# Kernel optimization log

Hardware: AMD Instinct MI355X
Metric: run time of the kernel (lower is better)

The kernel has to match this reference:

```python
import jax, jax.numpy as jnp
import numpy as np

HEAD_DIM = 64


def setup_inputs() -> dict:
    key = jax.random.key(0)
    ks = jax.random.split(key, 7)
    B, T, S = 8, 256, 4096
    E, KV = 512, 768          # embed_dim, kv_dim
    H, D = 8, HEAD_DIM        # num_heads, head_dim
    x = jax.random.normal(ks[0], (B, T, E), dtype=jnp.float32)
    context = jax.random.normal(ks[1], (B, S, KV), dtype=jnp.float32)
    key_padding_mask = jax.random.randint(ks[2], (B, S), 0, 2) > 0  # True = ignore
    Wq = jax.random.normal(ks[3], (H * D, E), dtype=jnp.float32) * 0.02
    Wkv = jax.random.normal(ks[4], (2 * H * D, KV), dtype=jnp.float32) * 0.02
    Wo = jax.random.normal(ks[5], (E, H * D), dtype=jnp.float32) * 0.02
    bo = jnp.zeros((E,), dtype=jnp.float32)
    return {"x": x, "context": context, "key_padding_mask": key_padding_mask,
            "Wq": Wq, "Wkv": Wkv, "Wo": Wo, "bo": bo}


def reference(x, context, key_padding_mask, Wq, Wkv, Wo, bo):
    B, T, _ = x.shape
    S = context.shape[1]
    D = HEAD_DIM
    H = Wq.shape[0] // D
    scale = D ** (-0.5)

    # q: (B, H, T, D)
    q = (x @ Wq.T).reshape(B, T, H, D).transpose(0, 2, 1, 3)
    # kv: (B, S, 2, H, D) -> k, v each (B, H, S, D)
    kv = (context @ Wkv.T).reshape(B, S, 2, H, D)
    k = kv[:, :, 0].transpose(0, 2, 1, 3)
    v = kv[:, :, 1].transpose(0, 2, 1, 3)

    # attention scores (B, H, T, S) -- materialized, matching att_weights capture
    attn = jnp.einsum('bhtd,bhsd->bhts', q, k) * scale
    attn = jnp.where(key_padding_mask[:, None, None, :], -jnp.inf, attn)
    attn = jax.nn.softmax(attn, axis=-1)  # dropout p=0.0 -> identity

    out = jnp.einsum('bhts,bhsd->bthd', attn, v).reshape(B, T, H * D)
    return out @ Wo.T + bo
```

## Files before the change

### kernel.cpp

```cpp
#include <hip/hip_runtime.h>
#include <hip/hip_bf16.h>


typedef float f32x4 __attribute__((ext_vector_type(4)));
typedef __bf16 bf16x8 __attribute__((ext_vector_type(8)));
typedef unsigned short u16x8 __attribute__((ext_vector_type(8)));
typedef unsigned short u16x4 __attribute__((ext_vector_type(4)));
typedef unsigned int u32x4 __attribute__((ext_vector_type(4)));

static __device__ __forceinline__ unsigned short f2bf(float f) {
  return __builtin_bit_cast(unsigned short, (__bf16)f);
}
static __device__ __forceinline__ unsigned pk2(float lo, float hi) {
  return (unsigned)f2bf(lo) | ((unsigned)f2bf(hi) << 16);
}
static __device__ __forceinline__ f32x4 mfma16(bf16x8 a, bf16x8 b, f32x4 c) {
  return __builtin_amdgcn_mfma_f32_16x16x32_bf16(a, b, c, 0, 0, 0);
}
static __device__ __forceinline__ bf16x8 ld_frag(const unsigned short* lds, int byteOff) {
  return __builtin_bit_cast(bf16x8, *(const u16x8*)((const char*)lds + byteOff));
}
static __device__ __forceinline__ void gll16(const void* g, void* l) {
  __builtin_amdgcn_global_load_lds((__attribute__((address_space(1))) void*)(void*)g,
                                   (__attribute__((address_space(3))) void*)l, 16, 0, 0);
}
static __device__ __forceinline__ int swz4(int row) {
  return (row + (row >> 1)) & 3;
}

__global__ __launch_bounds__(256) void cvt_ctx(const float* __restrict__ in,
                                               unsigned short* __restrict__ out) {
  const long t = blockIdx.x * 256L + threadIdx.x;
  f32x4 v[12];
#pragma unroll
  for (int it = 0; it < 6; ++it) {
    const f32x4* p = (const f32x4*)(in + (t + it * 524288L) * 8);
    v[it * 2] = p[0];
    v[it * 2 + 1] = p[1];
  }
#pragma unroll
  for (int it = 0; it < 6; ++it) {
    f32x4 a = v[it * 2], b = v[it * 2 + 1];
    u16x8 o = { f2bf(a[0]), f2bf(a[1]), f2bf(a[2]), f2bf(a[3]),
                f2bf(b[0]), f2bf(b[1]), f2bf(b[2]), f2bf(b[3]) };
    *(u16x8*)(out + (t + it * 524288L) * 8) = o;
  }
}

__global__ __launch_bounds__(256) void cvt_bf16(const float* __restrict__ in,
                                                unsigned short* __restrict__ out, int n8) {
  int i = blockIdx.x * 256 + threadIdx.x;
  if (i >= n8) return;
  const f32x4* p = (const f32x4*)(in + (long)i * 8);
  f32x4 a = p[0], b = p[1];
  u16x8 o = { f2bf(a[0]), f2bf(a[1]), f2bf(a[2]), f2bf(a[3]),
              f2bf(b[0]), f2bf(b[1]), f2bf(b[2]), f2bf(b[3]) };
  *(u16x8*)(out + (long)i * 8) = o;
}

__global__ __launch_bounds__(256) void gemm_kv(
    const unsigned short* __restrict__ A, const unsigned short* __restrict__ Bw,
    unsigned short* __restrict__ kbuf, unsigned short* __restrict__ vbuf) {
  constexpr int K = 768;
  constexpr int NT = K / 32;
  __shared__ unsigned short SH[24576];
  auto AsP = [&](int b) { return SH + b * 4096; };
  auto BsP = [&](int b) { return SH + 12288 + b * 4096; };
  const int tid = threadIdx.x;
  const int l = tid & 63, wid = tid >> 6;
  const int wr = wid >> 1, wc = wid & 1;
  const int r = l & 15, g = l >> 4;
  const int bid = blockIdx.x;
  const int xcd = bid & 7, j = bid >> 3;
  const long m0 = (long)(xcd * 32 + (j >> 3)) * 128;
  const long n0 = (long)(j & 7) * 128;

  const int row0 = tid >> 2, cs = tid & 3;
  const int gk0 = (cs ^ swz4(row0)) * 8;
  const unsigned short* aR = A + (m0 + row0) * K + gk0;
  const unsigned short* bR = Bw + (n0 + row0) * K + gk0;

  auto stage = [&](int sbuf, int kt) {
    const unsigned short* ap = aR + kt * 32;
    const unsigned short* bp = bR + kt * 32;
    gll16(ap,          (char*)AsP(sbuf) + tid * 16);
    gll16(ap + 64 * K, (char*)AsP(sbuf) + 4096 + tid * 16);
    gll16(bp,          (char*)BsP(sbuf) + tid * 16);
    gll16(bp + 64 * K, (char*)BsP(sbuf) + 4096 + tid * 16);
  };

  f32x4 acc[4][4] = {};
  stage(0, 0);
  stage(1, 1);
  asm volatile("s_waitcnt vmcnt(4)" ::: "memory");
  __builtin_amdgcn_s_barrier();
  __builtin_amdgcn_sched_barrier(0);

  int cur = 0, nxt2 = 2;
  for (int t = 0; t < NT; ++t) {
    if (t + 2 < NT) stage(nxt2, t + 2);
    bf16x8 af[4], bfr[4];
#pragma unroll
    for (int m = 0; m < 4; ++m) {
      int row = wr * 64 + m * 16 + r;
      af[m] = ld_frag(AsP(cur), row * 64 + ((g ^ swz4(row)) << 4));
    }
#pragma unroll
    for (int n = 0; n < 4; ++n) {
      int row = wc * 64 + n * 16 + r;
      bfr[n] = ld_frag(BsP(cur), row * 64 + ((g ^ swz4(row)) << 4));
    }
    __builtin_amdgcn_s_setprio(1);
#pragma unroll
    for (int m = 0; m < 4; ++m)
#pragma unroll
      for (int n = 0; n < 4; ++n)
        acc[m][n] = mfma16(af[m], bfr[n], acc[m][n]);
    __builtin_amdgcn_s_setprio(0);
    if (t + 2 < NT) {
      asm volatile("s_waitcnt vmcnt(4)" ::: "memory");
    } else {
      asm volatile("s_waitcnt vmcnt(0)" ::: "memory");
    }
    __builtin_amdgcn_s_barrier();
    __builtin_amdgcn_sched_barrier(0);
    cur = (cur == 2) ? 0 : cur + 1;
    nxt2 = (nxt2 == 2) ? 0 : nxt2 + 1;
  }

  const bool isK = (n0 < 512);
  unsigned short* ep = SH + wid * 4224;
#pragma unroll
  for (int m = 0; m < 4; ++m)
#pragma unroll
    for (int n = 0; n < 4; ++n)
#pragma unroll
      for (int i = 0; i < 4; ++i) {
        int lr = m * 16 + g * 4 + i;
        int lc = n * 16 + r;
        if (isK) ep[lr * 66 + lc] = f2bf(acc[m][n][i]);
        else     ep[lc * 66 + lr] = f2bf(acc[m][n][i]);
      }
  asm volatile("s_waitcnt lgkmcnt(0)" ::: "memory");

  const int rr0 = l >> 3, cch = l & 7;
  if (isK) {
    const int hh = (int)((n0 + wc * 64) >> 6);
    const long srow0 = m0 + wr * 64;
    const int bb = (int)(srow0 >> 12);
    unsigned short* kb = kbuf + ((long)(bb * 8 + hh) * 4096) * 64;
#pragma unroll
    for (int q = 0; q < 8; ++q) {
      int rr = q * 8 + rr0;
      u16x8 vv = *(const u16x8*)&ep[rr * 66 + cch * 8];
      int ss = (int)((srow0 + rr) & 4095);
      *(u16x8*)&kb[(long)ss * 64 + cch * 8] = vv;
    }
  } else {
    const int c2 = (int)(n0 - 512) + wc * 64;
    const int hh = c2 >> 6;
    const long srow0 = m0 + wr * 64;
    const int bb = (int)(srow0 >> 12), ss0 = (int)(srow0 & 4095);
    unsigned short* vb = vbuf + ((long)(bb * 8 + hh) * 64) * 4096;
#pragma unroll
    for (int q = 0; q < 8; ++q) {
      int dd = q * 8 + rr0;
      u16x8 vv = *(const u16x8*)&ep[dd * 66 + cch * 8];
      *(u16x8*)&vb[(long)dd * 4096 + ss0 + cch * 8] = vv;
    }
  }
}

template <int OUTMODE, typename TA>
__global__ __launch_bounds__(256) void gemm_bt(
    const TA* __restrict__ A, const float* __restrict__ Bw,
    int M, int N, int K,
    unsigned short* __restrict__ o16a,
    float* __restrict__ oF, const float* __restrict__ bias) {
  __shared__ unsigned short As[2][128 * 32];
  __shared__ unsigned short Bs[2][128 * 32];
  const int tid = threadIdx.x;
  const int l = tid & 63, wid = tid >> 6;
  const int wr = wid >> 1, wc = wid & 1;
  const int r = l & 15, g = l >> 4;
  const long m0 = (long)blockIdx.y * 128, n0 = (long)blockIdx.x * 128;

  const int srow = tid >> 1, sseg = tid & 1;
  const int sz = swz4(srow);
  const int wb0 = srow * 64 + (((sseg * 2) ^ sz) << 4);
  const int wb1 = srow * 64 + (((sseg * 2 + 1) ^ sz) << 4);

  const TA* aptr = A + (m0 + srow) * (long)K + sseg * 16;
  const float* bptr = Bw + (n0 + srow) * (long)K + sseg * 16;

  f32x4 rA[4]; u16x8 rAh[2]; f32x4 rB[4];
  auto loadT = [&](int kt) {
    if constexpr (sizeof(TA) == 4) {
      const f32x4* p = (const f32x4*)(aptr + kt * 32);
      rA[0] = p[0]; rA[1] = p[1]; rA[2] = p[2]; rA[3] = p[3];
    } else {
      const u16x8* p = (const u16x8*)(aptr + kt * 32);
      rAh[0] = p[0]; rAh[1] = p[1];
    }
    const f32x4* q = (const f32x4*)(bptr + kt * 32);
    rB[0] = q[0]; rB[1] = q[1]; rB[2] = q[2]; rB[3] = q[3];
  };
  auto writeT = [&](int sbuf) {
    char* ab = (char*)As[sbuf];
    if constexpr (sizeof(TA) == 4) {
      u32x4 lo = { pk2(rA[0][0], rA[0][1]), pk2(rA[0][2], rA[0][3]),
                   pk2(rA[1][0], rA[1][1]), pk2(rA[1][2], rA[1][3]) };
      u32x4 hi = { pk2(rA[2][0], rA[2][1]), pk2(rA[2][2], rA[2][3]),
                   pk2(rA[3][0], rA[3][1]), pk2(rA[3][2], rA[3][3]) };
      *(u32x4*)(ab + wb0) = lo; *(u32x4*)(ab + wb1) = hi;
    } else {
      *(u16x8*)(ab + wb0) = rAh[0]; *(u16x8*)(ab + wb1) = rAh[1];
    }
    char* bb = (char*)Bs[sbuf];
    u32x4 lo = { pk2(rB[0][0], rB[0][1]), pk2(rB[0][2], rB[0][3]),
                 pk2(rB[1][0], rB[1][1]), pk2(rB[1][2], rB[1][3]) };
    u32x4 hi = { pk2(rB[2][0], rB[2][1]), pk2(rB[2][2], rB[2][3]),
                 pk2(rB[3][0], rB[3][1]), pk2(rB[3][2], rB[3][3]) };
    *(u32x4*)(bb + wb0) = lo; *(u32x4*)(bb + wb1) = hi;
  };

  f32x4 acc[4][4] = {};
  const int nt = K >> 5;
  loadT(0); writeT(0);
  __syncthreads();
  int buf = 0;
  for (int t = 0; t < nt; ++t) {
    if (t + 1 < nt) loadT(t + 1);
    bf16x8 af[4], bfr[4];
#pragma unroll
    for (int m = 0; m < 4; ++m) {
      int row = wr * 64 + m * 16 + r;
      af[m] = ld_frag(As[buf], row * 64 + ((g ^ swz4(row)) << 4));
    }
#pragma unroll
    for (int n = 0; n < 4; ++n) {
      int row = wc * 64 + n * 16 + r;
      bfr[n] = ld_frag(Bs[buf], row * 64 + ((g ^ swz4(row)) << 4));
    }
#pragma unroll
    for (int m = 0; m < 4; ++m)
#pragma unroll
      for (int n = 0; n < 4; ++n)
        acc[m][n] = mfma16(af[m], bfr[n], acc[m][n]);
    if (t + 1 < nt) writeT(buf ^ 1);
    __syncthreads();
    buf ^= 1;
  }

#pragma unroll
  for (int m = 0; m < 4; ++m) {
#pragma unroll
    for (int n = 0; n < 4; ++n) {
      f32x4 v = acc[m][n];
      const long rg0 = m0 + wr * 64 + m * 16 + g * 4;
      const long cg = n0 + wc * 64 + n * 16 + r;
      if constexpr (OUTMODE == 0) {
#pragma unroll
        for (int i = 0; i < 4; ++i) {
          long rg = rg0 + i;
          int bb = (int)(rg >> 8), tt = (int)(rg & 255);
          int hh = (int)(cg >> 6), dd = (int)(cg & 63);
          o16a[(((long)(bb * 8 + hh) * 256 + tt) << 6) + dd] = f2bf(v[i]);
        }
      } else {
#pragma unroll
        for (int i = 0; i < 4; ++i) {
          long rg = rg0 + i;
          oF[rg * (long)N + cg] = v[i] + bias[cg];
        }
      }
    }
  }
}

__global__ __launch_bounds__(256) void attn_fwd(
    const unsigned short* __restrict__ qbuf,
    const unsigned short* __restrict__ kbuf,
    const unsigned short* __restrict__ vbuf,
    const int* __restrict__ mask,
    float* __restrict__ po, float* __restrict__ ml) {
  __shared__ unsigned short Ks[2][64 * 64];
  __shared__ unsigned short Vs[2][64 * 64];
  __shared__ unsigned short Ps[4][16 * 64];
  const int tid = threadIdx.x;
  const int l = tid & 63, w = tid >> 6;
  const int r = l & 15, g = l >> 4;
  const int bid = blockIdx.x;
  const int b = bid & 7;
  const int idx = bid >> 3;
  const int sp = idx >> 5, h = (idx >> 2) & 7, qt = idx & 3;
  const int bh = b * 8 + h;

  const unsigned short* qrow = qbuf + (((long)bh * 256) + qt * 64 + w * 16 + r) * 64;
  const bf16x8 qf0 = __builtin_bit_cast(bf16x8, *(const u16x8*)(qrow + g * 8));
  const bf16x8 qf1 = __builtin_bit_cast(bf16x8, *(const u16x8*)(qrow + 32 + g * 8));

  f32x4 accO[4] = {};
  float mrow[4] = { -1e30f, -1e30f, -1e30f, -1e30f };
  float lrow[4] = {};
  const float SCL = 0.125f * 1.44269504088896340736f;

  const int s_base = sp * 1024;
  const unsigned short* kbase = kbuf + ((long)bh * 4096 + s_base) * 64;
  const unsigned short* vbase = vbuf + ((long)bh * 64) * 4096 + s_base;
  const int* mbase = mask + b * 4096 + s_base;

  const int st_row = tid >> 3, st_c = tid & 7;
  auto stage = [&](int sbuf, int t0) {
#pragma unroll
    for (int p = 0; p < 2; ++p) {
      int row = p * 32 + st_row;
      int colb = (st_c * 16) ^ ((row & 7) << 4);
      int ldsOff = (p * 256 + tid) * 16;
      gll16(kbase + (long)(t0 + row) * 64 + (colb >> 1), (char*)Ks[sbuf] + ldsOff);
      gll16(vbase + (long)row * 4096 + t0 + (colb >> 1), (char*)Vs[sbuf] + ldsOff);
    }
  };

  stage(0, 0);
  asm volatile("s_waitcnt vmcnt(0)" ::: "memory");
  __builtin_amdgcn_s_barrier();
  __builtin_amdgcn_sched_barrier(0);

  int buf = 0;
  for (int it = 0; it < 16; ++it) {
    if (it + 1 < 16) stage(buf ^ 1, (it + 1) * 64);

    f32x4 sc[4] = {};
    __builtin_amdgcn_s_setprio(1);
#pragma unroll
    for (int nf = 0; nf < 4; ++nf) {
      int row = nf * 16 + r;
      int swz = (row & 7) << 4;
      bf16x8 k0 = ld_frag(Ks[buf], row * 128 + ((g * 16) ^ swz));
      bf16x8 k1 = ld_frag(Ks[buf], row * 128 + ((g * 16 + 64) ^ swz));
      sc[nf] = mfma16(qf0, k0, sc[nf]);
      sc[nf] = mfma16(qf1, k1, sc[nf]);
    }
    __builtin_amdgcn_s_setprio(0);

    float s[4][4];
#pragma unroll
    for (int nf = 0; nf < 4; ++nf) {
      bool mk = mbase[it * 64 + nf * 16 + r] != 0;
#pragma unroll
      for (int i = 0; i < 4; ++i) s[nf][i] = mk ? -1e30f : sc[nf][i] * SCL;
    }

    float tm[4], pr[4][4], rs[4], corr[4];
#pragma unroll
    for (int i = 0; i < 4; ++i) {
      tm[i] = fmaxf(fmaxf(s[0][i], s[1][i]), fmaxf(s[2][i], s[3][i]));
#pragma unroll
      for (int off = 1; off < 16; off <<= 1)
        tm[i] = fmaxf(tm[i], __shfl_xor(tm[i], off));
      float mn = fmaxf(mrow[i], tm[i]);
      corr[i] = exp2f(mrow[i] - mn);
      mrow[i] = mn;
      rs[i] = 0.f;
    }
#pragma unroll
    for (int nf = 0; nf < 4; ++nf)
#pragma unroll
      for (int i = 0; i < 4; ++i) {
        pr[nf][i] = exp2f(s[nf][i] - mrow[i]);
        rs[i] += pr[nf][i];
      }
#pragma unroll
    for (int i = 0; i < 4; ++i) {
#pragma unroll
      for (int off = 1; off < 16; off <<= 1)
        rs[i] += __shfl_xor(rs[i], off);
      lrow[i] = lrow[i] * corr[i] + rs[i];
    }
    f32x4 cv = { corr[0], corr[1], corr[2], corr[3] };
#pragma unroll
    for (int nf = 0; nf < 4; ++nf) accO[nf] *= cv;

    unsigned short* Pw = Ps[w];
#pragma unroll
    for (int nf = 0; nf < 4; ++nf)
#pragma unroll
      for (int i = 0; i < 4; ++i) {
        int prow = g * 4 + i;
        int pb = prow * 128 + ((((nf * 16 + r) * 2)) ^ ((prow & 7) << 4));
        *(unsigned short*)((char*)Pw + pb) = f2bf(pr[nf][i]);
      }
    asm volatile("s_waitcnt lgkmcnt(0)" ::: "memory");
    bf16x8 pf0 = ld_frag(Pw, r * 128 + ((g * 16) ^ ((r & 7) << 4)));
    bf16x8 pf1 = ld_frag(Pw, r * 128 + ((g * 16 + 64) ^ ((r & 7) << 4)));

    __builtin_amdgcn_s_setprio(1);
#pragma unroll
    for (int nf = 0; nf < 4; ++nf) {
      int row = nf * 16 + r;
      int swz = (row & 7) << 4;
      bf16x8 v0 = ld_frag(Vs[buf], row * 128 + ((g * 16) ^ swz));
      bf16x8 v1 = ld_frag(Vs[buf], row * 128 + ((g * 16 + 64) ^ swz));
      accO[nf] = mfma16(pf0, v0, accO[nf]);
      accO[nf] = mfma16(pf1, v1, accO[nf]);
    }
    __builtin_amdgcn_s_setprio(0);

    asm volatile("s_waitcnt vmcnt(0)" ::: "memory");
    __builtin_amdgcn_s_barrier();
    __builtin_amdgcn_sched_barrier(0);
    buf ^= 1;
  }

  const long rowg = (long)bh * 256 + qt * 64 + w * 16 + g * 4;
#pragma unroll
  for (int nf = 0; nf < 4; ++nf)
#pragma unroll
    for (int i = 0; i < 4; ++i)
      po[((long)sp * 16384 + rowg + i) * 64 + nf * 16 + r] = accO[nf][i];
  if (r == 0) {
#pragma unroll
    for (int i = 0; i < 4; ++i) {
      ml[((long)sp * 16384 + rowg + i) * 2 + 0] = mrow[i];
      ml[((long)sp * 16384 + rowg + i) * 2 + 1] = lrow[i];
    }
  }
}

__global__ __launch_bounds__(256) void attn_merge(
    const float* __restrict__ po, const float* __restrict__ ml,
    unsigned short* __restrict__ obuf) {
  const int idx = blockIdx.x * 256 + threadIdx.x;
  const int row = idx >> 2, dc = (idx & 3) << 4;
  float ms[4], ls[4], mx = -1e30f;
#pragma unroll
  for (int sp = 0; sp < 4; ++sp) {
    ms[sp] = ml[((long)sp * 16384 + row) * 2 + 0];
    ls[sp] = ml[((long)sp * 16384 + row) * 2 + 1];
    mx = fmaxf(mx, ms[sp]);
  }
  float lsum = 0.f, wg[4];
#pragma unroll
  for (int sp = 0; sp < 4; ++sp) { wg[sp] = exp2f(ms[sp] - mx); lsum += wg[sp] * ls[sp]; }
  const float inv = 1.f / lsum;
  f32x4 o[4] = {};
#pragma unroll
  for (int sp = 0; sp < 4; ++sp) {
    const f32x4* p = (const f32x4*)(po + ((long)sp * 16384 + row) * 64 + dc);
#pragma unroll
    for (int c = 0; c < 4; ++c) o[c] += wg[sp] * p[c];
  }
  u16x8 o0, o1;
#pragma unroll
  for (int k = 0; k < 8; ++k) {
    o0[k] = f2bf(o[k >> 2][k & 3] * inv);
    o1[k] = f2bf(o[2 + (k >> 2)][k & 3] * inv);
  }
  const long off = (((long)((row >> 11) * 256 + (row & 255))) << 9) + ((row >> 8) & 7) * 64 + dc;
  *(u16x8*)&obuf[off] = o0;
  *(u16x8*)&obuf[off + 8] = o1;
}

extern "C" void kernel_launch(void* const* d_in, const int* in_sizes, int n_in,
                              void* d_out, int out_size, void* d_ws, size_t ws_size,
                              hipStream_t stream) {
  (void)in_sizes; (void)n_in; (void)out_size; (void)ws_size;
  const float* x    = (const float*)d_in[0];
  const float* ctx  = (const float*)d_in[1];
  const int*   mask = (const int*)d_in[2];
  const float* Wq   = (const float*)d_in[3];
  const float* Wkv  = (const float*)d_in[4];
  const float* Wo   = (const float*)d_in[5];
  const float* bo   = (const float*)d_in[6];
  float* out = (float*)d_out;

  char* ws = (char*)d_ws;
  const size_t MiB = 1024 * 1024;
  unsigned short* kbuf = (unsigned short*)(ws);
  unsigned short* vbuf = (unsigned short*)(ws + 32 * MiB);
  unsigned short* ctxb = (unsigned short*)(ws + 64 * MiB);
  unsigned short* qbuf = (unsigned short*)(ws + 64 * MiB);
  unsigned short* obuf = (unsigned short*)(ws + 66 * MiB);
  float* po = (float*)(ws + 68 * MiB);
  float* ml = (float*)(ws + 84 * MiB);
  unsigned short* wkvb = (unsigned short*)(ws + 112 * MiB);

  cvt_ctx<<<dim3(2048), 256, 0, stream>>>(ctx, ctxb);
  cvt_bf16<<<dim3(384), 256, 0, stream>>>(Wkv, wkvb, 98304);
  gemm_kv<<<dim3(2048), 256, 0, stream>>>(ctxb, wkvb, kbuf, vbuf);
  gemm_bt<0, float><<<dim3(4, 16), 256, 0, stream>>>(
      x, Wq, 2048, 512, 512, qbuf, nullptr, nullptr);
  attn_fwd<<<dim3(1024), 256, 0, stream>>>(qbuf, kbuf, vbuf, mask, po, ml);
  attn_merge<<<dim3(256), 256, 0, stream>>>(po, ml, obuf);
  gemm_bt<2, unsigned short><<<dim3(4, 16), 256, 0, stream>>>(
      obuf, Wo, 2048, 512, 512, nullptr, out, bo);
}
```

Before: 192.7 us.

## Enlarge KV projection GEMM tiles to 256x256 with 8 waves and split staging

```diff
diff --git a/kernel.cpp b/kernel.cpp
--- a/kernel.cpp
+++ b/kernel.cpp
@@ -58,115 +58,125 @@
   *(u16x8*)(out + (long)i * 8) = o;
 }
 
-__global__ __launch_bounds__(256) void gemm_kv(
+__global__ __launch_bounds__(512) void gemm_kv(
     const unsigned short* __restrict__ A, const unsigned short* __restrict__ Bw,
     unsigned short* __restrict__ kbuf, unsigned short* __restrict__ vbuf) {
   constexpr int K = 768;
   constexpr int NT = K / 32;
-  __shared__ unsigned short SH[24576];
-  auto AsP = [&](int b) { return SH + b * 4096; };
-  auto BsP = [&](int b) { return SH + 12288 + b * 4096; };
+  __shared__ unsigned short SH[49152];
+  auto AsP = [&](int b) { return SH + b * 8192; };
+  auto BsP = [&](int b) { return SH + 24576 + b * 8192; };
   const int tid = threadIdx.x;
   const int l = tid & 63, wid = tid >> 6;
-  const int wr = wid >> 1, wc = wid & 1;
+  const int wr = wid >> 2, wc = wid & 3;
   const int r = l & 15, g = l >> 4;
   const int bid = blockIdx.x;
   const int xcd = bid & 7, j = bid >> 3;
-  const long m0 = (long)(xcd * 32 + (j >> 3)) * 128;
-  const long n0 = (long)(j & 7) * 128;
-
-  const int row0 = tid >> 2, cs = tid & 3;
-  const int gk0 = (cs ^ swz4(row0)) * 8;
-  const unsigned short* aR = A + (m0 + row0) * K + gk0;
-  const unsigned short* bR = Bw + (n0 + row0) * K + gk0;
-
-  auto stage = [&](int sbuf, int kt) {
-    const unsigned short* ap = aR + kt * 32;
-    const unsigned short* bp = bR + kt * 32;
-    gll16(ap,          (char*)AsP(sbuf) + tid * 16);
-    gll16(ap + 64 * K, (char*)AsP(sbuf) + 4096 + tid * 16);
-    gll16(bp,          (char*)BsP(sbuf) + tid * 16);
-    gll16(bp + 64 * K, (char*)BsP(sbuf) + 4096 + tid * 16);
+  const long m0 = (long)(xcd * 16 + (j >> 2)) * 256;
+  const long n0 = (long)(j & 3) * 256;
+
+  const int rl = tid >> 2, cs = tid & 3;
+  const int gk0 = (cs ^ swz4(rl)) * 8;
+  const unsigned short* aR = A + (m0 + rl) * K + gk0;
+  const unsigned short* bR = Bw + (n0 + rl) * K + gk0;
+
+  auto halfstage = [&](int sbuf, int kt, int hs) {
+    char* ab = (char*)AsP(sbuf);
+    char* bb = (char*)BsP(sbuf);
+    if (hs == 0)      gll16(aR + kt * 32,           ab + tid * 16);
+    else if (hs == 1) gll16(aR + 128 * K + kt * 32, ab + 8192 + tid * 16);
+    else if (hs == 2) gll16(bR + kt * 32,           bb + tid * 16);
+    else              gll16(bR + 128 * K + kt * 32, bb + 8192 + tid * 16);
   };
 
-  f32x4 acc[4][4] = {};
-  stage(0, 0);
-  stage(1, 1);
+  f32x4 acc[8][4] = {};
+
+  for (int hs = 0; hs < 4; ++hs) halfstage(0, 0, hs);
+  for (int hs = 0; hs < 4; ++hs) halfstage(1, 1, hs);
   asm volatile("s_waitcnt vmcnt(4)" ::: "memory");
   __builtin_amdgcn_s_barrier();
   __builtin_amdgcn_sched_barrier(0);
 
   int cur = 0, nxt2 = 2;
   for (int t = 0; t < NT; ++t) {
-    if (t + 2 < NT) stage(nxt2, t + 2);
-    bf16x8 af[4], bfr[4];
-#pragma unroll
-    for (int m = 0; m < 4; ++m) {
-      int row = wr * 64 + m * 16 + r;
-      af[m] = ld_frag(AsP(cur), row * 64 + ((g ^ swz4(row)) << 4));
-    }
-#pragma unroll
-    for (int n = 0; n < 4; ++n) {
-      int row = wc * 64 + n * 16 + r;
-      bfr[n] = ld_frag(BsP(cur), row * 64 + ((g ^ swz4(row)) << 4));
-    }
-    __builtin_amdgcn_s_setprio(1);
-#pragma unroll
-    for (int m = 0; m < 4; ++m)
-#pragma unroll
-      for (int n = 0; n < 4; ++n)
-        acc[m][n] = mfma16(af[m], bfr[n], acc[m][n]);
-    __builtin_amdgcn_s_setprio(0);
-    if (t + 2 < NT) {
-      asm volatile("s_waitcnt vmcnt(4)" ::: "memory");
-    } else {
-      asm volatile("s_waitcnt vmcnt(0)" ::: "memory");
-    }
-    __builtin_amdgcn_s_barrier();
-    __builtin_amdgcn_sched_barrier(0);
+    const unsigned short* Ab = AsP(cur);
+    const unsigned short* Bb = BsP(cur);
+    const bool st = (t + 2 < NT);
+#pragma unroll
+    for (int q = 0; q < 4; ++q) {
+      const int qm = q >> 1, qn = q & 1;
+      bf16x8 af[4], bfv[2];
+#pragma unroll
+      for (int i = 0; i < 4; ++i) {
+        int row = wr * 128 + (qm * 4 + i) * 16 + r;
+        af[i] = ld_frag(Ab, row * 64 + ((g ^ swz4(row)) << 4));
+      }
+#pragma unroll
+      for (int jn = 0; jn < 2; ++jn) {
+        int row = wc * 64 + (qn * 2 + jn) * 16 + r;
+        bfv[jn] = ld_frag(Bb, row * 64 + ((g ^ swz4(row)) << 4));
+      }
+      if (st) halfstage(nxt2, t + 2, q);
+      __builtin_amdgcn_s_setprio(1);
+#pragma unroll
+      for (int i = 0; i < 4; ++i)
+#pragma unroll
+        for (int jn = 0; jn < 2; ++jn)
+          acc[qm * 4 + i][qn * 2 + jn] =
+              mfma16(af[i], bfv[jn], acc[qm * 4 + i][qn * 2 + jn]);
+      __builtin_amdgcn_s_setprio(0);
+      if (q == 3) {
+        if (st) { asm volatile("s_waitcnt vmcnt(4)" ::: "memory"); }
+        else    { asm volatile("s_waitcnt vmcnt(0)" ::: "memory"); }
+      }
+      __builtin_amdgcn_s_barrier();
+      __builtin_amdgcn_sched_barrier(0);
+    }
     cur = (cur == 2) ? 0 : cur + 1;
     nxt2 = (nxt2 == 2) ? 0 : nxt2 + 1;
   }
 
   const bool isK = (n0 < 512);
   unsigned short* ep = SH + wid * 4224;
-#pragma unroll
-  for (int m = 0; m < 4; ++m)
-#pragma unroll
-    for (int n = 0; n < 4; ++n)
-#pragma unroll
-      for (int i = 0; i < 4; ++i) {
-        int lr = m * 16 + g * 4 + i;
-        int lc = n * 16 + r;
-        if (isK) ep[lr * 66 + lc] = f2bf(acc[m][n][i]);
-        else     ep[lc * 66 + lr] = f2bf(acc[m][n][i]);
-      }
-  asm volatile("s_waitcnt lgkmcnt(0)" ::: "memory");
-
   const int rr0 = l >> 3, cch = l & 7;
-  if (isK) {
-    const int hh = (int)((n0 + wc * 64) >> 6);
-    const long srow0 = m0 + wr * 64;
-    const int bb = (int)(srow0 >> 12);
-    unsigned short* kb = kbuf + ((long)(bb * 8 + hh) * 4096) * 64;
-#pragma unroll
-    for (int q = 0; q < 8; ++q) {
-      int rr = q * 8 + rr0;
-      u16x8 vv = *(const u16x8*)&ep[rr * 66 + cch * 8];
-      int ss = (int)((srow0 + rr) & 4095);
-      *(u16x8*)&kb[(long)ss * 64 + cch * 8] = vv;
-    }
-  } else {
-    const int c2 = (int)(n0 - 512) + wc * 64;
-    const int hh = c2 >> 6;
-    const long srow0 = m0 + wr * 64;
-    const int bb = (int)(srow0 >> 12), ss0 = (int)(srow0 & 4095);
-    unsigned short* vb = vbuf + ((long)(bb * 8 + hh) * 64) * 4096;
-#pragma unroll
-    for (int q = 0; q < 8; ++q) {
-      int dd = q * 8 + rr0;
-      u16x8 vv = *(const u16x8*)&ep[dd * 66 + cch * 8];
-      *(u16x8*)&vb[(long)dd * 4096 + ss0 + cch * 8] = vv;
+#pragma unroll
+  for (int sr = 0; sr < 2; ++sr) {
+    if (sr == 1) { asm volatile("s_waitcnt lgkmcnt(0)" ::: "memory"); }
+#pragma unroll
+    for (int mm = 0; mm < 4; ++mm)
+#pragma unroll
+      for (int n = 0; n < 4; ++n)
+#pragma unroll
+        for (int i = 0; i < 4; ++i) {
+          int lr = mm * 16 + g * 4 + i;
+          int lc = n * 16 + r;
+          if (isK) ep[lr * 66 + lc] = f2bf(acc[sr * 4 + mm][n][i]);
+          else     ep[lc * 66 + lr] = f2bf(acc[sr * 4 + mm][n][i]);
+        }
+    asm volatile("s_waitcnt lgkmcnt(0)" ::: "memory");
+    const long srow0 = m0 + wr * 128 + sr * 64;
+    if (isK) {
+      const int hh = (int)((n0 + wc * 64) >> 6);
+      const int bb = (int)(srow0 >> 12);
+      unsigned short* kb = kbuf + ((long)(bb * 8 + hh) * 4096) * 64;
+#pragma unroll
+      for (int q2 = 0; q2 < 8; ++q2) {
+        int rr = q2 * 8 + rr0;
+        u16x8 vv = *(const u16x8*)&ep[rr * 66 + cch * 8];
+        int ss = (int)((srow0 + rr) & 4095);
+        *(u16x8*)&kb[(long)ss * 64 + cch * 8] = vv;
+      }
+    } else {
+      const int c2 = (int)(n0 - 512) + wc * 64;
+      const int hh = c2 >> 6;
+      const int bb = (int)(srow0 >> 12), ss0 = (int)(srow0 & 4095);
+      unsigned short* vb = vbuf + ((long)(bb * 8 + hh) * 64) * 4096;
+#pragma unroll
+      for (int q2 = 0; q2 < 8; ++q2) {
+        int dd = q2 * 8 + rr0;
+        u16x8 vv = *(const u16x8*)&ep[dd * 66 + cch * 8];
+        *(u16x8*)&vb[(long)dd * 4096 + ss0 + cch * 8] = vv;
+      }
     }
   }
 }
@@ -488,7 +498,7 @@
 
   cvt_ctx<<<dim3(2048), 256, 0, stream>>>(ctx, ctxb);
   cvt_bf16<<<dim3(384), 256, 0, stream>>>(Wkv, wkvb, 98304);
-  gemm_kv<<<dim3(2048), 256, 0, stream>>>(ctxb, wkvb, kbuf, vbuf);
+  gemm_kv<<<dim3(512), 512, 0, stream>>>(ctxb, wkvb, kbuf, vbuf);
   gemm_bt<0, float><<<dim3(4, 16), 256, 0, stream>>>(
       x, Wq, 2048, 512, 512, qbuf, nullptr, nullptr);
   attn_fwd<<<dim3(1024), 256, 0, stream>>>(qbuf, kbuf, vbuf, mask, po, ml);
```

New measurement: 198.4 us. +2.9%, slower.

## Fuse conversions and Q projection into one prep kernel; load KV weights directly to registers

Applied to the files above, without the earlier changes.

```diff
diff --git a/kernel.cpp b/kernel.cpp
--- a/kernel.cpp
+++ b/kernel.cpp
@@ -28,44 +28,130 @@
   return (row + (row >> 1)) & 3;
 }
 
-__global__ __launch_bounds__(256) void cvt_ctx(const float* __restrict__ in,
-                                               unsigned short* __restrict__ out) {
-  const long t = blockIdx.x * 256L + threadIdx.x;
-  f32x4 v[12];
-#pragma unroll
-  for (int it = 0; it < 6; ++it) {
-    const f32x4* p = (const f32x4*)(in + (t + it * 524288L) * 8);
-    v[it * 2] = p[0];
-    v[it * 2 + 1] = p[1];
-  }
-#pragma unroll
-  for (int it = 0; it < 6; ++it) {
-    f32x4 a = v[it * 2], b = v[it * 2 + 1];
+__global__ __launch_bounds__(256) void prep(
+    const float* __restrict__ ctx, unsigned short* __restrict__ ctxb,
+    const float* __restrict__ Wkv, unsigned short* __restrict__ wkvb,
+    const float* __restrict__ x, const float* __restrict__ Wq,
+    unsigned short* __restrict__ qbuf) {
+  __shared__ unsigned short As[2][128 * 32];
+  __shared__ unsigned short Bs[2][128 * 32];
+  const int bidx = blockIdx.x;
+  const int tid = threadIdx.x;
+
+  if (bidx < 2048) {
+    const long t = bidx * 256L + tid;
+    f32x4 v[12];
+#pragma unroll
+    for (int it = 0; it < 6; ++it) {
+      const f32x4* p = (const f32x4*)(ctx + (t + it * 524288L) * 8);
+      v[it * 2] = p[0];
+      v[it * 2 + 1] = p[1];
+    }
+#pragma unroll
+    for (int it = 0; it < 6; ++it) {
+      f32x4 a = v[it * 2], b = v[it * 2 + 1];
+      u16x8 o = { f2bf(a[0]), f2bf(a[1]), f2bf(a[2]), f2bf(a[3]),
+                  f2bf(b[0]), f2bf(b[1]), f2bf(b[2]), f2bf(b[3]) };
+      *(u16x8*)(ctxb + (t + it * 524288L) * 8) = o;
+    }
+    return;
+  }
+  if (bidx < 2432) {
+    const long i = (bidx - 2048) * 256L + tid;
+    const f32x4* p = (const f32x4*)(Wkv + i * 8);
+    f32x4 a = p[0], b = p[1];
     u16x8 o = { f2bf(a[0]), f2bf(a[1]), f2bf(a[2]), f2bf(a[3]),
                 f2bf(b[0]), f2bf(b[1]), f2bf(b[2]), f2bf(b[3]) };
-    *(u16x8*)(out + (t + it * 524288L) * 8) = o;
-  }
-}
-
-__global__ __launch_bounds__(256) void cvt_bf16(const float* __restrict__ in,
-                                                unsigned short* __restrict__ out, int n8) {
-  int i = blockIdx.x * 256 + threadIdx.x;
-  if (i >= n8) return;
-  const f32x4* p = (const f32x4*)(in + (long)i * 8);
-  f32x4 a = p[0], b = p[1];
-  u16x8 o = { f2bf(a[0]), f2bf(a[1]), f2bf(a[2]), f2bf(a[3]),
-              f2bf(b[0]), f2bf(b[1]), f2bf(b[2]), f2bf(b[3]) };
-  *(u16x8*)(out + (long)i * 8) = o;
+    *(u16x8*)(wkvb + i * 8) = o;
+    return;
+  }
+
+  constexpr int K = 512;
+  const int qb = bidx - 2432;
+  const long m0 = (long)(qb >> 2) * 128, n0 = (long)(qb & 3) * 128;
+  const int l = tid & 63, wid = tid >> 6;
+  const int wr = wid >> 1, wc = wid & 1;
+  const int r = l & 15, g = l >> 4;
+  const int srow = tid >> 1, sseg = tid & 1;
+  const int sz = swz4(srow);
+  const int wb0 = srow * 64 + (((sseg * 2) ^ sz) << 4);
+  const int wb1 = srow * 64 + (((sseg * 2 + 1) ^ sz) << 4);
+  const float* aptr = x + (m0 + srow) * (long)K + sseg * 16;
+  const float* bptr = Wq + (n0 + srow) * (long)K + sseg * 16;
+
+  f32x4 rA[4]; f32x4 rB[4];
+  auto loadT = [&](int kt) {
+    const f32x4* p = (const f32x4*)(aptr + kt * 32);
+    rA[0] = p[0]; rA[1] = p[1]; rA[2] = p[2]; rA[3] = p[3];
+    const f32x4* q = (const f32x4*)(bptr + kt * 32);
+    rB[0] = q[0]; rB[1] = q[1]; rB[2] = q[2]; rB[3] = q[3];
+  };
+  auto writeT = [&](int sbuf) {
+    char* ab = (char*)As[sbuf];
+    u32x4 lo = { pk2(rA[0][0], rA[0][1]), pk2(rA[0][2], rA[0][3]),
+                 pk2(rA[1][0], rA[1][1]), pk2(rA[1][2], rA[1][3]) };
+    u32x4 hi = { pk2(rA[2][0], rA[2][1]), pk2(rA[2][2], rA[2][3]),
+                 pk2(rA[3][0], rA[3][1]), pk2(rA[3][2], rA[3][3]) };
+    *(u32x4*)(ab + wb0) = lo; *(u32x4*)(ab + wb1) = hi;
+    char* bb = (char*)Bs[sbuf];
+    u32x4 lo2 = { pk2(rB[0][0], rB[0][1]), pk2(rB[0][2], rB[0][3]),
+                  pk2(rB[1][0], rB[1][1]), pk2(rB[1][2], rB[1][3]) };
+    u32x4 hi2 = { pk2(rB[2][0], rB[2][1]), pk2(rB[2][2], rB[2][3]),
+                  pk2(rB[3][0], rB[3][1]), pk2(rB[3][2], rB[3][3]) };
+    *(u32x4*)(bb + wb0) = lo2; *(u32x4*)(bb + wb1) = hi2;
+  };
+
+  f32x4 acc[4][4] = {};
+  const int nt = K >> 5;
+  loadT(0); writeT(0);
+  __syncthreads();
+  int buf = 0;
+  for (int t = 0; t < nt; ++t) {
+    if (t + 1 < nt) loadT(t + 1);
+    bf16x8 af[4], bfr[4];
+#pragma unroll
+    for (int m = 0; m < 4; ++m) {
+      int row = wr * 64 + m * 16 + r;
+      af[m] = ld_frag(As[buf], row * 64 + ((g ^ swz4(row)) << 4));
+    }
+#pragma unroll
+    for (int n = 0; n < 4; ++n) {
+      int row = wc * 64 + n * 16 + r;
+      bfr[n] = ld_frag(Bs[buf], row * 64 + ((g ^ swz4(row)) << 4));
+    }
+#pragma unroll
+    for (int m = 0; m < 4; ++m)
+#pragma unroll
+      for (int n = 0; n < 4; ++n)
+        acc[m][n] = mfma16(af[m], bfr[n], acc[m][n]);
+    if (t + 1 < nt) writeT(buf ^ 1);
+    __syncthreads();
+    buf ^= 1;
+  }
+#pragma unroll
+  for (int m = 0; m < 4; ++m)
+#pragma unroll
+    for (int n = 0; n < 4; ++n) {
+      f32x4 v = acc[m][n];
+      const long rg0 = m0 + wr * 64 + m * 16 + g * 4;
+      const long cg = n0 + wc * 64 + n * 16 + r;
+#pragma unroll
+      for (int i = 0; i < 4; ++i) {
+        long rg = rg0 + i;
+        int bb = (int)(rg >> 8), tt = (int)(rg & 255);
+        int hh = (int)(cg >> 6), dd = (int)(cg & 63);
+        qbuf[(((long)(bb * 8 + hh) * 256 + tt) << 6) + dd] = f2bf(v[i]);
+      }
+    }
 }
 
 __global__ __launch_bounds__(256) void gemm_kv(
     const unsigned short* __restrict__ A, const unsigned short* __restrict__ Bw,
     unsigned short* __restrict__ kbuf, unsigned short* __restrict__ vbuf) {
   constexpr int K = 768;
-  constexpr int NT = K / 32;
-  __shared__ unsigned short SH[24576];
+  constexpr int NT = 24;
+  __shared__ unsigned short SH[16896];
   auto AsP = [&](int b) { return SH + b * 4096; };
-  auto BsP = [&](int b) { return SH + 12288 + b * 4096; };
   const int tid = threadIdx.x;
   const int l = tid & 63, wid = tid >> 6;
   const int wr = wid >> 1, wc = wid & 1;
@@ -78,47 +164,57 @@
   const int row0 = tid >> 2, cs = tid & 3;
   const int gk0 = (cs ^ swz4(row0)) * 8;
   const unsigned short* aR = A + (m0 + row0) * K + gk0;
-  const unsigned short* bR = Bw + (n0 + row0) * K + gk0;
-
-  auto stage = [&](int sbuf, int kt) {
+  const unsigned short* bBase = Bw + (n0 + wc * 64 + r) * (long)K + g * 8;
+
+  auto stageA = [&](int sbuf, int kt) {
     const unsigned short* ap = aR + kt * 32;
-    const unsigned short* bp = bR + kt * 32;
     gll16(ap,          (char*)AsP(sbuf) + tid * 16);
     gll16(ap + 64 * K, (char*)AsP(sbuf) + 4096 + tid * 16);
-    gll16(bp,          (char*)BsP(sbuf) + tid * 16);
-    gll16(bp + 64 * K, (char*)BsP(sbuf) + 4096 + tid * 16);
+  };
+  u16x8 bc[4], bn[4];
+  auto loadBc = [&](int kt) {
+#pragma unroll
+    for (int n = 0; n < 4; ++n)
+      bc[n] = *(const u16x8*)(bBase + (long)n * 16 * K + kt * 32);
+  };
+  auto loadBn = [&](int kt) {
+#pragma unroll
+    for (int n = 0; n < 4; ++n)
+      bn[n] = *(const u16x8*)(bBase + (long)n * 16 * K + kt * 32);
   };
 
   f32x4 acc[4][4] = {};
-  stage(0, 0);
-  stage(1, 1);
-  asm volatile("s_waitcnt vmcnt(4)" ::: "memory");
+  loadBc(0);
+  stageA(0, 0);
+  stageA(1, 1);
+  loadBn(1);
+  asm volatile("s_waitcnt vmcnt(6)" ::: "memory");
   __builtin_amdgcn_s_barrier();
   __builtin_amdgcn_sched_barrier(0);
 
   int cur = 0, nxt2 = 2;
   for (int t = 0; t < NT; ++t) {
-    if (t + 2 < NT) stage(nxt2, t + 2);
-    bf16x8 af[4], bfr[4];
+    if (t + 2 < NT) stageA(nxt2, t + 2);
+    bf16x8 af[4];
 #pragma unroll
     for (int m = 0; m < 4; ++m) {
       int row = wr * 64 + m * 16 + r;
       af[m] = ld_frag(AsP(cur), row * 64 + ((g ^ swz4(row)) << 4));
     }
-#pragma unroll
-    for (int n = 0; n < 4; ++n) {
-      int row = wc * 64 + n * 16 + r;
-      bfr[n] = ld_frag(BsP(cur), row * 64 + ((g ^ swz4(row)) << 4));
-    }
     __builtin_amdgcn_s_setprio(1);
 #pragma unroll
     for (int m = 0; m < 4; ++m)
 #pragma unroll
       for (int n = 0; n < 4; ++n)
-        acc[m][n] = mfma16(af[m], bfr[n], acc[m][n]);
+        acc[m][n] = mfma16(af[m], __builtin_bit_cast(bf16x8, bc[n]), acc[m][n]);
     __builtin_amdgcn_s_setprio(0);
+    if (t + 1 < NT) {
+#pragma unroll
+      for (int n = 0; n < 4; ++n) bc[n] = bn[n];
+      if (t + 2 < NT) loadBn(t + 2);
+    }
     if (t + 2 < NT) {
-      asm volatile("s_waitcnt vmcnt(4)" ::: "memory");
+      asm volatile("s_waitcnt vmcnt(6)" ::: "memory");
     } else {
       asm volatile("s_waitcnt vmcnt(0)" ::: "memory");
     }
@@ -465,7 +561,7 @@
 extern "C" void kernel_launch(void* const* d_in, const int* in_sizes, int n_in,
                               void* d_out, int out_size, void* d_ws, size_t ws_size,
                               hipStream_t stream) {
-  (void)in_sizes; (void)n_in; (void)out_size; (void)ws_size;
+  (void)in_sizes; (void)n_in; (void)out_size;
   const float* x    = (const float*)d_in[0];
   const float* ctx  = (const float*)d_in[1];
   const int*   mask = (const int*)d_in[2];
@@ -480,17 +576,22 @@
   unsigned short* kbuf = (unsigned short*)(ws);
   unsigned short* vbuf = (unsigned short*)(ws + 32 * MiB);
   unsigned short* ctxb = (unsigned short*)(ws + 64 * MiB);
-  unsigned short* qbuf = (unsigned short*)(ws + 64 * MiB);
   unsigned short* obuf = (unsigned short*)(ws + 66 * MiB);
   float* po = (float*)(ws + 68 * MiB);
   float* ml = (float*)(ws + 84 * MiB);
   unsigned short* wkvb = (unsigned short*)(ws + 112 * MiB);
 
-  cvt_ctx<<<dim3(2048), 256, 0, stream>>>(ctx, ctxb);
-  cvt_bf16<<<dim3(384), 256, 0, stream>>>(Wkv, wkvb, 98304);
+  const bool fuseQ = ws_size >= (size_t)(115 * MiB + 512 * 1024);
+  unsigned short* qbuf = fuseQ
+      ? (unsigned short*)(ws + 113 * MiB + 512 * 1024)
+      : (unsigned short*)(ws + 64 * MiB);
+
+  prep<<<dim3(fuseQ ? 2496 : 2432), 256, 0, stream>>>(
+      ctx, ctxb, Wkv, wkvb, x, Wq, qbuf);
   gemm_kv<<<dim3(2048), 256, 0, stream>>>(ctxb, wkvb, kbuf, vbuf);
-  gemm_bt<0, float><<<dim3(4, 16), 256, 0, stream>>>(
-      x, Wq, 2048, 512, 512, qbuf, nullptr, nullptr);
+  if (!fuseQ)
+    gemm_bt<0, float><<<dim3(4, 16), 256, 0, stream>>>(
+        x, Wq, 2048, 512, 512, qbuf, nullptr, nullptr);
   attn_fwd<<<dim3(1024), 256, 0, stream>>>(qbuf, kbuf, vbuf, mask, po, ml);
   attn_merge<<<dim3(256), 256, 0, stream>>>(po, ml, obuf);
   gemm_bt<2, unsigned short><<<dim3(4, 16), 256, 0, stream>>>(
```

Result: slower. 237.3 us (+23.1%).
